# Performance work log

Hardware: AMD Instinct MI355X
Metric: run time of the kernel (lower is better)

Reference implementation:

```python
import jax, jax.numpy as jnp
import numpy as np

N_NODES = 50000
N_EDGES = 800000
D = 64
EPS = 1e-12  # torch F.normalize eps


def edge_softmax(e, dst, n):
    # softmax over incoming edges of each dst node, per feature channel
    m = jax.ops.segment_max(e, dst, num_segments=n)          # [N, D]
    ex = jnp.exp(e - m[dst])                                 # [E, D]
    s = jax.ops.segment_sum(ex, dst, num_segments=n)         # [N, D]
    return ex / s[dst]


def gat_layer(h, src, dst, W_src, b_src, W_dst, b_dst, n):
    # attention logits: u_mul_v
    e = h[src] * h[dst]                                      # [E, D]
    alpha = edge_softmax(e, dst, n)                          # [E, D]
    # transformed features (fc_dst computed in source but unused downstream)
    feat_src = jax.nn.relu(h @ W_src.T + b_src)              # [N, D]
    _feat_dst = jax.nn.relu(h @ W_dst.T + b_dst)             # [N, D] (dead, kept for fidelity)
    # message: u_mul_e, then scatter-sum to dst
    msg = feat_src[src] * alpha                              # [E, D]
    return jax.ops.segment_sum(msg, dst, num_segments=n)     # [N, D]


def l2_normalize(x):
    nrm = jnp.sqrt(jnp.sum(x * x, axis=1, keepdims=True))
    return x / jnp.maximum(nrm, EPS)


def setup_inputs() -> dict:
    key = jax.random.key(0)
    ks = jax.random.split(key, 10)
    scale = 1.0 / np.sqrt(D)
    return {
        "node_ids": jax.random.randint(ks[0], (N_NODES,), 0, N_NODES),
        "src": jax.random.randint(ks[1], (N_EDGES,), 0, N_NODES),
        "dst": jax.random.randint(ks[2], (N_EDGES,), 0, N_NODES),
        "embed_table": jax.random.normal(ks[3], (N_NODES, D), jnp.float32) * 0.1,
        "W_src_0": jax.random.normal(ks[4], (D, D), jnp.float32) * scale,
        "b_src_0": jnp.zeros((D,), jnp.float32),
        "W_dst_0": jax.random.normal(ks[5], (D, D), jnp.float32) * scale,
        "b_dst_0": jnp.zeros((D,), jnp.float32),
        "W_src_1": jax.random.normal(ks[6], (D, D), jnp.float32) * scale,
        "b_src_1": jnp.zeros((D,), jnp.float32),
        "W_dst_1": jax.random.normal(ks[7], (D, D), jnp.float32) * scale,
        "b_dst_1": jnp.zeros((D,), jnp.float32),
    }


def reference(node_ids, src, dst, embed_table,
              W_src_0, b_src_0, W_dst_0, b_dst_0,
              W_src_1, b_src_1, W_dst_1, b_dst_1):
    n = node_ids.shape[0]
    h0 = embed_table[node_ids]                               # [N, D]
    h1 = gat_layer(h0, src, dst, W_src_0, b_src_0, W_dst_0, b_dst_0, n)
    h2 = gat_layer(h1, src, dst, W_src_1, b_src_1, W_dst_1, b_dst_1, n)
    # cache = [h0, norm(h1), norm(h2)]; h passed forward unnormalized
    return jnp.concatenate([h0, l2_normalize(h1), l2_normalize(h2)], axis=1)  # [N, 3D]
```

## Files before the change

kernel.cpp:

```cpp
#include <hip/hip_runtime.h>
#include <math.h>

#define NN 50000
#define NE 800000
#define DD 64

typedef __attribute__((ext_vector_type(8))) short short8v;
typedef __attribute__((ext_vector_type(4))) float floatx4;

__device__ __forceinline__ unsigned bf16r(float x) {
  unsigned u = __float_as_uint(x);
  return (u + 0x7fffu + ((u >> 16) & 1u)) >> 16;
}


__global__ void k_prep(const float* __restrict__ emb, const int* __restrict__ ids,
                       const int* __restrict__ dst, float* __restrict__ out,
                       int* __restrict__ deg, int* __restrict__ pos) {
  int idx = blockIdx.x * 256 + threadIdx.x;
  if (idx < NN * DD) {
    int node = idx >> 6, d = idx & 63;
    out[node * 192 + d] = emb[ids[node] * DD + d];
  }
  if (idx < NE) pos[idx] = atomicAdd(&deg[dst[idx]], 1);
}

__global__ void k_scan1(const int* __restrict__ deg, int* __restrict__ rp,
                        int* __restrict__ bsum) {
  __shared__ int tmp[1024];
  int t = threadIdx.x;
  int i = blockIdx.x * 1024 + t;
  int v = (i < NN) ? deg[i] : 0;
  tmp[t] = v;
  __syncthreads();
  for (int off = 1; off < 1024; off <<= 1) {
    int x = (t >= off) ? tmp[t - off] : 0;
    __syncthreads();
    tmp[t] += x;
    __syncthreads();
  }
  if (i < NN) rp[i] = tmp[t] - v;
  if (t == 1023) bsum[blockIdx.x] = tmp[1023];
}

__global__ void k_scan2(int* __restrict__ bsum, int nb) {
  int t = threadIdx.x;
  int orig = (t < nb) ? bsum[t] : 0;
  int v = orig;
#pragma unroll
  for (int off = 1; off < 64; off <<= 1) {
    int x = __shfl_up(v, off, 64);
    if (t >= off) v += x;
  }
  if (t < nb) bsum[t] = v - orig;
}

__global__ void k_scan3(int* __restrict__ rp, const int* __restrict__ bsum) {
  int i = blockIdx.x * 1024 + threadIdx.x;
  if (i < NN) rp[i] += bsum[blockIdx.x];
  if (i == 0) rp[NN] = NE;
}

__global__ void k_scatter(const int* __restrict__ src, const int* __restrict__ dst,
                          const int* __restrict__ rp, const int* __restrict__ pos,
                          int* __restrict__ ssrc) {
  int e = blockIdx.x * 256 + threadIdx.x;
  if (e < NE) ssrc[rp[dst[e]] + pos[e]] = src[e];
}

__global__ void __launch_bounds__(256) k_fc_mfma(const float* __restrict__ h, int hstride,
                                                 const float* __restrict__ W,
                                                 const float* __restrict__ b,
                                                 unsigned* __restrict__ hfb) {
  int lane = threadIdx.x & 63;
  int wid = threadIdx.x >> 6;
  int nbase = blockIdx.x * 64 + wid * 16;
  if (nbase >= NN) return;
  int r16 = lane & 15, kg = lane >> 4;

  short8v afr[2];
  const float* hrow = h + (size_t)(nbase + r16) * hstride;
#pragma unroll
  for (int kt = 0; kt < 2; ++kt) {
    int k0 = kt * 32 + kg * 8;
#pragma unroll
    for (int i = 0; i < 8; ++i) afr[kt][i] = (short)bf16r(hrow[k0 + i]);
  }
  short8v bfr[4][2];
#pragma unroll
  for (int dt = 0; dt < 4; ++dt) {
    const float* wrow = W + (dt * 16 + r16) * 64;
#pragma unroll
    for (int kt = 0; kt < 2; ++kt) {
      int k0 = kt * 32 + kg * 8;
#pragma unroll
      for (int i = 0; i < 8; ++i) bfr[dt][kt][i] = (short)bf16r(wrow[k0 + i]);
    }
  }
#pragma unroll
  for (int dt = 0; dt < 4; ++dt) {
    floatx4 acc = {0.f, 0.f, 0.f, 0.f};
    acc = __builtin_amdgcn_mfma_f32_16x16x32_bf16(afr[0], bfr[dt][0], acc, 0, 0, 0);
    acc = __builtin_amdgcn_mfma_f32_16x16x32_bf16(afr[1], bfr[dt][1], acc, 0, 0, 0);
    int d = dt * 16 + r16;
    float bias = b[d];
#pragma unroll
    for (int r = 0; r < 4; ++r) {
      int node = nbase + kg * 4 + r;
      float feat = fmaxf(acc[r] + bias, 0.f);
      float hv = h[(size_t)node * hstride + d];
      hfb[node * DD + d] = bf16r(hv) | (bf16r(feat) << 16);
    }
  }
}

__global__ void __launch_bounds__(256) k_edge(const unsigned* __restrict__ hfb,
                                              const float* __restrict__ hsrc, int hstride,
                                              const int* __restrict__ rp,
                                              const int* __restrict__ ssrc,
                                              float* __restrict__ hout, int ostride) {
  int d = threadIdx.x & 63;
  int node = blockIdx.x * 4 + (threadIdx.x >> 6);
  if (node >= NN) return;
  int beg = rp[node], end = rp[node + 1];
  float hd = hsrc[node * hstride + d];
  float s0 = 0.f, s1 = 0.f, s2 = 0.f, s3 = 0.f;
  float s4 = 0.f, s5 = 0.f, s6 = 0.f, s7 = 0.f;
  float a0 = 0.f, a1 = 0.f, a2 = 0.f, a3 = 0.f;
  float a4 = 0.f, a5 = 0.f, a6 = 0.f, a7 = 0.f;
  int p = beg;
#define EDGE_STEP(j, sj, aj)                                        \
  {                                                                 \
    unsigned v = hfb[ssrc[p + j] * DD + d];                         \
    float hv = __uint_as_float(v << 16);                            \
    float fv = __uint_as_float(v & 0xffff0000u);                    \
    float ex = __expf(hv * hd);                                     \
    sj += ex;                                                       \
    aj = fmaf(fv, ex, aj);                                          \
  }
  for (; p + 8 <= end; p += 8) {
    EDGE_STEP(0, s0, a0) EDGE_STEP(1, s1, a1) EDGE_STEP(2, s2, a2) EDGE_STEP(3, s3, a3)
    EDGE_STEP(4, s4, a4) EDGE_STEP(5, s5, a5) EDGE_STEP(6, s6, a6) EDGE_STEP(7, s7, a7)
  }
  for (; p < end; ++p) EDGE_STEP(0, s0, a0)
#undef EDGE_STEP
  float s = ((s0 + s1) + (s2 + s3)) + ((s4 + s5) + (s6 + s7));
  float a = ((a0 + a1) + (a2 + a3)) + ((a4 + a5) + (a6 + a7));
  hout[node * ostride + d] = (end > beg) ? a / s : 0.f;
}

__global__ void __launch_bounds__(256) k_final(const float* __restrict__ h1,
                                               float* __restrict__ out) {
  int d = threadIdx.x & 63;
  int node = blockIdx.x * 4 + (threadIdx.x >> 6);
  if (node >= NN) return;
  float v1 = h1[node * DD + d], v2 = out[node * 192 + 128 + d];
  float s1 = v1 * v1, s2 = v2 * v2;
#pragma unroll
  for (int off = 32; off > 0; off >>= 1) {
    s1 += __shfl_xor(s1, off, 64);
    s2 += __shfl_xor(s2, off, 64);
  }
  out[node * 192 + 64 + d] = v1 / fmaxf(sqrtf(s1), 1e-12f);
  out[node * 192 + 128 + d] = v2 / fmaxf(sqrtf(s2), 1e-12f);
}


extern "C" void kernel_launch(void* const* d_in, const int* in_sizes, int n_in,
                              void* d_out, int out_size, void* d_ws, size_t ws_size,
                              hipStream_t stream) {
  const int* node_ids = (const int*)d_in[0];
  const int* src = (const int*)d_in[1];
  const int* dst = (const int*)d_in[2];
  const float* emb = (const float*)d_in[3];
  const float* W0 = (const float*)d_in[4];
  const float* b0 = (const float*)d_in[5];
  const float* W1 = (const float*)d_in[8];
  const float* b1 = (const float*)d_in[9];
  float* out = (float*)d_out;

  size_t o = 0;
  auto alloc = [&](size_t nbytes) {
    char* p = (char*)d_ws + o;
    o += (nbytes + 255) & ~(size_t)255;
    return (void*)p;
  };
  float* h1 = (float*)alloc((size_t)NN * DD * 4);
  unsigned* hfb = (unsigned*)alloc((size_t)NN * DD * 4);
  int* deg = (int*)alloc((size_t)NN * 4);
  int* rp = (int*)alloc((size_t)(NN + 1) * 4);
  int* bsum = (int*)alloc(64 * 4);
  int* ssrc = (int*)alloc((size_t)NE * 4);
  int* pos = (int*)alloc((size_t)NE * 4);
  (void)o; (void)ws_size; (void)in_sizes; (void)n_in; (void)out_size;

  hipMemsetAsync(deg, 0, (size_t)NN * 4, stream);

  k_prep<<<(NN * DD + 255) / 256, 256, 0, stream>>>(emb, node_ids, dst, out, deg, pos);
  int NB = (NN + 1023) / 1024;
  k_scan1<<<NB, 1024, 0, stream>>>(deg, rp, bsum);
  k_scan2<<<1, 64, 0, stream>>>(bsum, NB);
  k_scan3<<<NB, 1024, 0, stream>>>(rp, bsum);
  k_scatter<<<(NE + 255) / 256, 256, 0, stream>>>(src, dst, rp, pos, ssrc);

  k_fc_mfma<<<(NN + 63) / 64, 256, 0, stream>>>(out, 192, W0, b0, hfb);
  k_edge<<<(NN + 3) / 4, 256, 0, stream>>>(hfb, out, 192, rp, ssrc, h1, DD);
  k_fc_mfma<<<(NN + 63) / 64, 256, 0, stream>>>(h1, DD, W1, b1, hfb);
  k_edge<<<(NN + 3) / 4, 256, 0, stream>>>(hfb, h1, DD, rp, ssrc, out + 128, 192);

  k_final<<<(NN + 3) / 4, 256, 0, stream>>>(h1, out);
}
```

Baseline: 186.4 us.

## Gather embedding rows via node ids inside consumers instead of a prep copy

```diff
diff --git a/kernel.cpp b/kernel.cpp
--- a/kernel.cpp
+++ b/kernel.cpp
@@ -14,15 +14,10 @@
 }
 
 
-__global__ void k_prep(const float* __restrict__ emb, const int* __restrict__ ids,
-                       const int* __restrict__ dst, float* __restrict__ out,
-                       int* __restrict__ deg, int* __restrict__ pos) {
-  int idx = blockIdx.x * 256 + threadIdx.x;
-  if (idx < NN * DD) {
-    int node = idx >> 6, d = idx & 63;
-    out[node * 192 + d] = emb[ids[node] * DD + d];
-  }
-  if (idx < NE) pos[idx] = atomicAdd(&deg[dst[idx]], 1);
+__global__ void k_hist(const int* __restrict__ dst, int* __restrict__ deg,
+                       int* __restrict__ pos) {
+  int e = blockIdx.x * 256 + threadIdx.x;
+  if (e < NE) pos[e] = atomicAdd(&deg[dst[e]], 1);
 }
 
 __global__ void k_scan1(const int* __restrict__ deg, int* __restrict__ rp,
@@ -61,14 +56,20 @@
   if (i == 0) rp[NN] = NE;
 }
 
-__global__ void k_scatter(const int* __restrict__ src, const int* __restrict__ dst,
-                          const int* __restrict__ rp, const int* __restrict__ pos,
+__global__ void k_scatter(const int4* __restrict__ src4, const int4* __restrict__ dst4,
+                          const int* __restrict__ rp, const int4* __restrict__ pos4,
                           int* __restrict__ ssrc) {
-  int e = blockIdx.x * 256 + threadIdx.x;
-  if (e < NE) ssrc[rp[dst[e]] + pos[e]] = src[e];
-}
-
-__global__ void __launch_bounds__(256) k_fc_mfma(const float* __restrict__ h, int hstride,
+  int q = blockIdx.x * 256 + threadIdx.x;
+  if (q >= NE / 4) return;
+  int4 s = src4[q], dn = dst4[q], p = pos4[q];
+  ssrc[rp[dn.x] + p.x] = s.x;
+  ssrc[rp[dn.y] + p.y] = s.y;
+  ssrc[rp[dn.z] + p.z] = s.z;
+  ssrc[rp[dn.w] + p.w] = s.w;
+}
+
+__global__ void __launch_bounds__(256) k_fc_mfma(const float* __restrict__ h,
+                                                 const int* __restrict__ ids,
                                                  const float* __restrict__ W,
                                                  const float* __restrict__ b,
                                                  unsigned* __restrict__ hfb) {
@@ -78,13 +79,20 @@
   if (nbase >= NN) return;
   int r16 = lane & 15, kg = lane >> 4;
 
+  int rowA = ids ? ids[nbase + r16] : (nbase + r16);
+  const float* hrow = h + (size_t)rowA * DD;
   short8v afr[2];
-  const float* hrow = h + (size_t)(nbase + r16) * hstride;
 #pragma unroll
   for (int kt = 0; kt < 2; ++kt) {
     int k0 = kt * 32 + kg * 8;
 #pragma unroll
     for (int i = 0; i < 8; ++i) afr[kt][i] = (short)bf16r(hrow[k0 + i]);
+  }
+  int orow[4];
+#pragma unroll
+  for (int r = 0; r < 4; ++r) {
+    int node = nbase + kg * 4 + r;
+    orow[r] = ids ? ids[node] : node;
   }
   short8v bfr[4][2];
 #pragma unroll
@@ -108,14 +116,15 @@
     for (int r = 0; r < 4; ++r) {
       int node = nbase + kg * 4 + r;
       float feat = fmaxf(acc[r] + bias, 0.f);
-      float hv = h[(size_t)node * hstride + d];
+      float hv = h[(size_t)orow[r] * DD + d];
       hfb[node * DD + d] = bf16r(hv) | (bf16r(feat) << 16);
     }
   }
 }
 
 __global__ void __launch_bounds__(256) k_edge(const unsigned* __restrict__ hfb,
-                                              const float* __restrict__ hsrc, int hstride,
+                                              const float* __restrict__ h,
+                                              const int* __restrict__ ids,
                                               const int* __restrict__ rp,
                                               const int* __restrict__ ssrc,
                                               float* __restrict__ hout, int ostride) {
@@ -123,7 +132,8 @@
   int node = blockIdx.x * 4 + (threadIdx.x >> 6);
   if (node >= NN) return;
   int beg = rp[node], end = rp[node + 1];
-  float hd = hsrc[node * hstride + d];
+  int hrow = ids ? ids[node] : node;
+  float hd = h[(size_t)hrow * DD + d];
   float s0 = 0.f, s1 = 0.f, s2 = 0.f, s3 = 0.f;
   float s4 = 0.f, s5 = 0.f, s6 = 0.f, s7 = 0.f;
   float a0 = 0.f, a1 = 0.f, a2 = 0.f, a3 = 0.f;
@@ -149,7 +159,9 @@
   hout[node * ostride + d] = (end > beg) ? a / s : 0.f;
 }
 
-__global__ void __launch_bounds__(256) k_final(const float* __restrict__ h1,
+__global__ void __launch_bounds__(256) k_final(const float* __restrict__ emb,
+                                               const int* __restrict__ ids,
+                                               const float* __restrict__ h1,
                                                float* __restrict__ out) {
   int d = threadIdx.x & 63;
   int node = blockIdx.x * 4 + (threadIdx.x >> 6);
@@ -161,6 +173,7 @@
     s1 += __shfl_xor(s1, off, 64);
     s2 += __shfl_xor(s2, off, 64);
   }
+  out[node * 192 + d] = emb[(size_t)ids[node] * DD + d];
   out[node * 192 + 64 + d] = v1 / fmaxf(sqrtf(s1), 1e-12f);
   out[node * 192 + 128 + d] = v2 / fmaxf(sqrtf(s2), 1e-12f);
 }
@@ -196,17 +209,18 @@
 
   hipMemsetAsync(deg, 0, (size_t)NN * 4, stream);
 
-  k_prep<<<(NN * DD + 255) / 256, 256, 0, stream>>>(emb, node_ids, dst, out, deg, pos);
+  k_hist<<<(NE + 255) / 256, 256, 0, stream>>>(dst, deg, pos);
   int NB = (NN + 1023) / 1024;
   k_scan1<<<NB, 1024, 0, stream>>>(deg, rp, bsum);
   k_scan2<<<1, 64, 0, stream>>>(bsum, NB);
   k_scan3<<<NB, 1024, 0, stream>>>(rp, bsum);
-  k_scatter<<<(NE + 255) / 256, 256, 0, stream>>>(src, dst, rp, pos, ssrc);
-
-  k_fc_mfma<<<(NN + 63) / 64, 256, 0, stream>>>(out, 192, W0, b0, hfb);
-  k_edge<<<(NN + 3) / 4, 256, 0, stream>>>(hfb, out, 192, rp, ssrc, h1, DD);
-  k_fc_mfma<<<(NN + 63) / 64, 256, 0, stream>>>(h1, DD, W1, b1, hfb);
-  k_edge<<<(NN + 3) / 4, 256, 0, stream>>>(hfb, h1, DD, rp, ssrc, out + 128, 192);
-
-  k_final<<<(NN + 3) / 4, 256, 0, stream>>>(h1, out);
-}
+  k_scatter<<<(NE / 4 + 255) / 256, 256, 0, stream>>>(
+      (const int4*)src, (const int4*)dst, rp, (const int4*)pos, ssrc);
+
+  k_fc_mfma<<<(NN + 63) / 64, 256, 0, stream>>>(emb, node_ids, W0, b0, hfb);
+  k_edge<<<(NN + 3) / 4, 256, 0, stream>>>(hfb, emb, node_ids, rp, ssrc, h1, DD);
+  k_fc_mfma<<<(NN + 63) / 64, 256, 0, stream>>>(h1, nullptr, W1, b1, hfb);
+  k_edge<<<(NN + 3) / 4, 256, 0, stream>>>(hfb, h1, nullptr, rp, ssrc, out + 128, 192);
+
+  k_final<<<(NN + 3) / 4, 256, 0, stream>>>(emb, node_ids, h1, out);
+}
```

Result: no change. 187.5 us (+0.6%).
